# Optimization experiments

Measured on AMD Instinct MI355X. Metric: run time of the kernel, lower is better.

The kernel has to match this reference:

```python
import jax, jax.numpy as jnp
import numpy as np
import itertools

# --- constants matching init_kwargs / chosen problem size ---
MOD = 6.283185307179586       # 2*pi, modular wrap for angular error
DEG_U = 90.0                  # deg_u
DEG_P = 1.0                   # deg_p (grid resolution in degrees)
D = 4                         # number of active sources (ones per label row)
NUM_CLASSES = 181             # angle grid size
BATCH = 131072

# All D! permutations as one-hot matrices: exact LAP solution by brute force
# (equivalent to lap.lapjv on the square DxD cost matrix).
_PERMS = np.array(list(itertools.permutations(range(D))), dtype=np.int32)   # (D!, D)
PERM_OH = jnp.asarray(np.eye(D, dtype=np.float32)[_PERMS])                  # (D!, D, D)


def setup_inputs() -> dict:
    key = jax.random.key(0)
    k1, k2 = jax.random.split(key)
    # predicted DOAs live in the first D slots of logits (radians)
    logits = jax.random.normal(k1, (BATCH, NUM_CLASSES), dtype=jnp.float32)
    # labels: exactly D ones per row (D distinct grid indices)
    scores = jax.random.uniform(k2, (BATCH, NUM_CLASSES))
    idx = jnp.argsort(scores, axis=1)[:, :D]                     # D distinct cols per row
    labels = jnp.zeros((BATCH, NUM_CLASSES), dtype=jnp.int32)
    labels = labels.at[jnp.arange(BATCH)[:, None], idx].set(1)
    return {"logits": logits, "labels": labels}


def _sq_mod_diff(a, b):
    # ((a - b + mod/2) % mod - mod/2)**2 : squared wrapped angular error
    d = jnp.mod(a - b + MOD / 2, MOD) - MOD / 2
    return d * d


def reference(logits, labels):
    # np.where(labels==1)[0] returns ascending indices of the ones.
    # Stable ascending argsort of a 0/1 row puts the one-indices (in ascending
    # order) in the last D slots.
    one_idx = jnp.argsort(labels, axis=1)[:, -D:]                        # (B, D)
    label_ang = (one_idx.astype(jnp.float32) * DEG_P - DEG_U) * (jnp.pi / 180.0)  # (B, D) radians

    doa = logits[:, :D]                                                  # (B, D)
    # per-sample DxD cost matrix of squared modular errors
    cost = _sq_mod_diff(doa[:, :, None], label_ang[:, None, :])          # (B, D, D)
    # optimal assignment = min total cost over all permutations (exact LAP)
    totals = jnp.einsum('bij,pij->bp', cost, PERM_OH)                    # (B, D!)
    min_total = jnp.min(totals, axis=1)                                  # (B,)
    rmse = jnp.sqrt(min_total / D)                                       # (B,)
    return rmse.mean()
```

## Files before the change

### kernel.cpp

```cpp
#include <hip/hip_runtime.h>
#include <hip/hip_bf16.h>
#include <math.h>

constexpr int   NC      = 181;
constexpr int   BATCH   = 131072;
constexpr float MODC    = 6.2831853071795864769f;
constexpr float HALFMOD = 3.1415926535897932385f;
constexpr float DEG2RAD = 0.017453292519943295f;

__device__ __forceinline__ float sq_mod_diff(float x) {
    float t = x + HALFMOD;
    float m = t - floorf(t * (1.0f / MODC)) * MODC;
    float d = m - HALFMOD;
    return d * d;
}

constexpr int RPW = 32;
constexpr int CH  = 8;

__global__ __launch_bounds__(256) void rmspe_kernel(
    const float* __restrict__ logits,
    const int*   __restrict__ labels,
    float*       __restrict__ out)
{
    const int lane    = threadIdx.x & 63;
    const int waveBlk = threadIdx.x >> 6;
    const int gwave   = blockIdx.x * 4 + waveBlk;
    const int rowBase = gwave * RPW;

    float d0 = 0.f, d1 = 0.f, d2 = 0.f, d3 = 0.f;
    if (lane < RPW) {
        const float* lp = logits + (size_t)(rowBase + lane) * NC;
        d0 = lp[0]; d1 = lp[1]; d2 = lp[2]; d3 = lp[3];
    }

    int pk = 0;

    for (int c = 0; c < RPW; c += CH) {
        int b0[CH], b1[CH], b2[CH];
        #pragma unroll
        for (int j = 0; j < CH; ++j) {
            const size_t b = (size_t)(rowBase + c + j) * NC;
            b0[j] = labels[b + lane];
            b1[j] = labels[b + 64 + lane];
            b2[j] = (lane < NC - 128) ? labels[b + 128 + lane] : 0;
        }
        #pragma unroll
        for (int j = 0; j < CH; ++j) {
            unsigned long long m0 = __ballot(b0[j] != 0);
            unsigned long long m1 = __ballot(b1[j] != 0);
            unsigned long long m2 = __ballot(b2[j] != 0);
            int p[4];
            #pragma unroll
            for (int t = 0; t < 4; ++t) {
                if (m0)      { p[t] =       __builtin_ctzll(m0); m0 &= m0 - 1; }
                else if (m1) { p[t] = 64  + __builtin_ctzll(m1); m1 &= m1 - 1; }
                else         { p[t] = 128 + __builtin_ctzll(m2); m2 &= m2 - 1; }
            }
            const int pack = p[0] | (p[1] << 8) | (p[2] << 16) | (p[3] << 24);
            pk = (lane == c + j) ? pack : pk;
        }
    }

    float sum = 0.0f;
    if (lane < RPW) {
        float ang[4], doa[4] = {d0, d1, d2, d3};
        #pragma unroll
        for (int t = 0; t < 4; ++t) {
            const int p = (pk >> (8 * t)) & 0xFF;
            ang[t] = ((float)p - 90.0f) * DEG2RAD;
        }

        float cst[4][4];
        #pragma unroll
        for (int i = 0; i < 4; ++i)
            #pragma unroll
            for (int j = 0; j < 4; ++j)
                cst[i][j] = sq_mod_diff(doa[i] - ang[j]);

        float best = 1e30f;
        #pragma unroll
        for (int a = 0; a < 4; ++a) {
            #pragma unroll
            for (int b = 0; b < 4; ++b) {
                if (b == a) continue;
                const float top = cst[0][a] + cst[1][b];
                #pragma unroll
                for (int e = 0; e < 4; ++e) {
                    if (e == a || e == b) continue;
                    const int f = 6 - a - b - e;
                    best = fminf(best, top + cst[2][e] + cst[3][f]);
                }
            }
        }
        sum = sqrtf(best * 0.25f);
    }

    #pragma unroll
    for (int off = 32; off > 0; off >>= 1)
        sum += __shfl_down(sum, off);

    __shared__ float wsum[4];
    if (lane == 0) wsum[waveBlk] = sum;
    __syncthreads();
    if (threadIdx.x == 0) {
        float t = (wsum[0] + wsum[1]) + (wsum[2] + wsum[3]);
        atomicAdd(out, t * (1.0f / (float)BATCH));
    }
}

extern "C" void kernel_launch(void* const* d_in, const int* in_sizes, int n_in,
                              void* d_out, int out_size, void* d_ws, size_t ws_size,
                              hipStream_t stream) {
    const float* logits = (const float*)d_in[0];
    const int*   labels = (const int*)d_in[1];
    float*       out    = (float*)d_out;

    hipMemsetAsync(out, 0, sizeof(float), stream);

    rmspe_kernel<<<BATCH / (4 * RPW), 256, 0, stream>>>(logits, labels, out);
}
```

Before: 201.8 us.

## Load each wave's label block as contiguous int4 vectors and decode positions by ballot

Each wave now handles 16 rows. It treats their labels as one contiguous block of ints and reads it with coalesced 16-byte int4 loads, all issued up front, instead of three scalar per-row loads per chunk. Set-bit positions come from ballots over the vector components. A wave-uniform loop then maps each flat index to a (row, class) pair with a magic-number division and packs it into the owning lane. This aims to raise memory-level parallelism and bandwidth use on the dominant labels read, and the grid doubles as a result. The cost is a serial per-set-bit scalar loop and more registers held per lane.

```diff
diff --git a/kernel.cpp b/kernel.cpp
--- a/kernel.cpp
+++ b/kernel.cpp
@@ -15,8 +15,11 @@
     return d * d;
 }
 
-constexpr int RPW = 32;
-constexpr int CH  = 8;
+constexpr int RPW    = 16;
+constexpr int WINTS  = RPW * NC;
+constexpr int NFULL  = WINTS / 256;
+constexpr int TAILV  = (WINTS - NFULL * 256) / 4;
+constexpr unsigned MAGIC181 = 23729102u;
 
 __global__ __launch_bounds__(256) void rmspe_kernel(
     const float* __restrict__ logits,
@@ -34,31 +37,42 @@
         d0 = lp[0]; d1 = lp[1]; d2 = lp[2]; d3 = lp[3];
     }
 
-    int pk = 0;
+    const int4* p4 = (const int4*)(labels + (size_t)gwave * WINTS);
+    int4 data[NFULL + 1];
+    #pragma unroll
+    for (int k = 0; k < NFULL; ++k)
+        data[k] = p4[(size_t)k * 64 + lane];
+    {
+        int4 t = {0, 0, 0, 0};
+        if (lane < TAILV) t = p4[(size_t)NFULL * 64 + lane];
+        data[NFULL] = t;
+    }
 
-    for (int c = 0; c < RPW; c += CH) {
-        int b0[CH], b1[CH], b2[CH];
+    int pk  = 0;
+    int cnt = 0;
+
+    #pragma unroll
+    for (int k = 0; k < NFULL + 1; ++k) {
+        const int4 v = data[k];
+        unsigned long long m[4];
+        m[0] = __ballot(v.x != 0);
+        m[1] = __ballot(v.y != 0);
+        m[2] = __ballot(v.z != 0);
+        m[3] = __ballot(v.w != 0);
         #pragma unroll
-        for (int j = 0; j < CH; ++j) {
-            const size_t b = (size_t)(rowBase + c + j) * NC;
-            b0[j] = labels[b + lane];
-            b1[j] = labels[b + 64 + lane];
-            b2[j] = (lane < NC - 128) ? labels[b + 128 + lane] : 0;
-        }
-        #pragma unroll
-        for (int j = 0; j < CH; ++j) {
-            unsigned long long m0 = __ballot(b0[j] != 0);
-            unsigned long long m1 = __ballot(b1[j] != 0);
-            unsigned long long m2 = __ballot(b2[j] != 0);
-            int p[4];
-            #pragma unroll
-            for (int t = 0; t < 4; ++t) {
-                if (m0)      { p[t] =       __builtin_ctzll(m0); m0 &= m0 - 1; }
-                else if (m1) { p[t] = 64  + __builtin_ctzll(m1); m1 &= m1 - 1; }
-                else         { p[t] = 128 + __builtin_ctzll(m2); m2 &= m2 - 1; }
+        for (int c = 0; c < 4; ++c) {
+            unsigned long long mm = m[c];
+            while (mm) {
+                const int j = __builtin_ctzll(mm);
+                mm &= mm - 1;
+                const unsigned g   = 256u * k + 4u * j + c;
+                const unsigned row = __umulhi(g, MAGIC181);
+                const unsigned cls = g - 181u * row;
+                const bool mine = ((unsigned)lane == row);
+                const int  sh   = (cnt & 3) * 8;
+                pk  = mine ? (pk | ((int)cls << sh)) : pk;
+                cnt = mine ? (cnt + 1) : cnt;
             }
-            const int pack = p[0] | (p[1] << 8) | (p[2] << 16) | (p[3] << 24);
-            pk = (lane == c + j) ? pack : pk;
         }
     }
 
```

Result: faster. 192.1 us (-4.8%).
